# Kernel optimization log

Hardware: AMD Instinct MI355X
Metric: run time of the kernel (lower is better)

The kernel has to match this reference:

```python
import jax, jax.numpy as jnp
import numpy as np

B, T, D = 2, 2048, 2048
H, HD = 32, 64  # n_heads, head_dim; H*HD == attn_dim == D


def _rope(x, cos, sin):
    # x: (B,T,H,HD) with interleaved (real, imag) pairs on last dim
    b, t, h, hd = x.shape
    x2 = x.reshape(b, t, h, hd // 2, 2)
    xr, xi = x2[..., 0], x2[..., 1]
    c = cos[None, :, None, :]  # (1,T,1,HD/2)
    s = sin[None, :, None, :]
    out_r = xr * c - xi * s
    out_i = xr * s + xi * c
    return jnp.stack([out_r, out_i], axis=-1).reshape(b, t, h, hd)


def setup_inputs() -> dict:
    key = jax.random.key(0)
    ks = jax.random.split(key, 5)
    x = jax.random.normal(ks[0], (B, T, D), dtype=jnp.float32)
    scale = 0.02
    wq = jax.random.normal(ks[1], (D, D), dtype=jnp.float32) * scale
    wk = jax.random.normal(ks[2], (D, D), dtype=jnp.float32) * scale
    wv = jax.random.normal(ks[3], (D, D), dtype=jnp.float32) * scale
    wo = jax.random.normal(ks[4], (D, D), dtype=jnp.float32) * scale
    # standard RoPE frequencies, theta = 10000
    inv_freq = 1.0 / (10000.0 ** (jnp.arange(0, HD, 2, dtype=jnp.float32) / HD))  # (HD/2,)
    angles = jnp.arange(T, dtype=jnp.float32)[:, None] * inv_freq[None, :]  # (T, HD/2)
    return {
        "x": x,
        "freqs_cos": jnp.cos(angles),
        "freqs_sin": jnp.sin(angles),
        "wq": wq, "wk": wk, "wv": wv, "wo": wo,
    }


def reference(x, freqs_cos, freqs_sin, wq, wk, wv, wo):
    b, t, d = x.shape
    # fused-style QKV projections (nn.Linear: x @ W.T, no bias)
    q = (x @ wq.T).reshape(b, t, H, HD)
    k = (x @ wk.T).reshape(b, t, H, HD)
    v = (x @ wv.T).reshape(b, t, H, HD)
    q = _rope(q, freqs_cos, freqs_sin)
    k = _rope(k, freqs_cos, freqs_sin)
    # causal SDPA, scale = 1/sqrt(head_dim)
    scale = 1.0 / jnp.sqrt(jnp.float32(HD))
    scores = jnp.einsum("bqhd,bkhd->bhqk", q, k) * scale  # (B,H,T,T)
    causal = jnp.tril(jnp.ones((t, t), dtype=bool))
    scores = jnp.where(causal[None, None], scores, jnp.float32(-jnp.inf))
    attn = jax.nn.softmax(scores, axis=-1)
    y = jnp.einsum("bhqk,bkhd->bqhd", attn, v).reshape(b, t, H * HD)
    return y @ wo.T
```

## Files before the change

### kernel.cpp

```cpp
#include <hip/hip_runtime.h>
#include <hip/hip_bf16.h>
#include <stdint.h>


typedef __bf16 bf16_t;
typedef __bf16 bf16x4 __attribute__((ext_vector_type(4)));
typedef __bf16 bf16x8 __attribute__((ext_vector_type(8)));
typedef float  f32x4  __attribute__((ext_vector_type(4)));

constexpr int B_ = 2, T_ = 2048, D_ = 2048, H_ = 32, HD_ = 64;
constexpr int M_ = B_ * T_;

__device__ __forceinline__ void async_copy16(const bf16_t* g, bf16_t* l) {
  __builtin_amdgcn_global_load_lds(
      (const __attribute__((address_space(1))) void*)g,
      (__attribute__((address_space(3))) void*)l, 16, 0, 0);
}

__global__ __launch_bounds__(256) void cast_f32_bf16(
    const float* __restrict__ src, bf16_t* __restrict__ dst, int n4)
{
  const int i = blockIdx.x * 256 + threadIdx.x;
  if (i >= n4) return;
  const float4 v = ((const float4*)src)[i];
  bf16x4 o;
  o[0] = (bf16_t)v.x; o[1] = (bf16_t)v.y; o[2] = (bf16_t)v.z; o[3] = (bf16_t)v.w;
  ((bf16x4*)dst)[i] = o;
}

template <typename OutT>
__global__ __launch_bounds__(256, 2) void gemm_bt(
    const bf16_t* __restrict__ A, const bf16_t* __restrict__ B,
    OutT* __restrict__ C, int M, int N, int K)
{
  __shared__ __attribute__((aligned(16))) bf16_t As[128 * 32];
  __shared__ __attribute__((aligned(16))) bf16_t Bs[128 * 32];

  const int tid    = threadIdx.x;
  const int w      = tid >> 6;
  const int l      = tid & 63;
  const int quad   = l >> 4;
  const int lane16 = l & 15;
  const int bm0 = blockIdx.x * 128;
  const int bn0 = blockIdx.y * 128;
  const int wm  = (w >> 1) * 64;
  const int wn  = (w & 1) * 64;
  const int srow = l >> 2;
  const int scol = (l & 3) * 8;

  const bf16_t* Ag = A + (size_t)bm0 * K;
  const bf16_t* Bg = B + (size_t)bn0 * K;

  f32x4 acc[4][4] = {};

  for (int kk = 0; kk < K; kk += 32) {
    __syncthreads();
#pragma unroll
    for (int s0 = 0; s0 < 2; ++s0) {
      const int s = w + s0 * 4;
      async_copy16(Ag + (size_t)(s * 16 + srow) * K + kk + scol, &As[s * 512]);
      async_copy16(Bg + (size_t)(s * 16 + srow) * K + kk + scol, &Bs[s * 512]);
    }
    __syncthreads();

    bf16x8 af[4], bfr[4];
#pragma unroll
    for (int i = 0; i < 4; ++i)
      af[i] = *(const bf16x8*)&As[(wm + i * 16 + lane16) * 32 + quad * 8];
#pragma unroll
    for (int j = 0; j < 4; ++j)
      bfr[j] = *(const bf16x8*)&Bs[(wn + j * 16 + lane16) * 32 + quad * 8];
#pragma unroll
    for (int i = 0; i < 4; ++i)
#pragma unroll
      for (int j = 0; j < 4; ++j)
        acc[i][j] = __builtin_amdgcn_mfma_f32_16x16x32_bf16(af[i], bfr[j],
                                                            acc[i][j], 0, 0, 0);
  }

#pragma unroll
  for (int i = 0; i < 4; ++i) {
#pragma unroll
    for (int r = 0; r < 4; ++r) {
      const size_t row = (size_t)(bm0 + wm + i * 16 + quad * 4 + r);
#pragma unroll
      for (int j = 0; j < 4; ++j) {
        const int col = bn0 + wn + j * 16 + lane16;
        C[row * N + col] = (OutT)acc[i][j][r];
      }
    }
  }
}

__global__ __launch_bounds__(256, 2) void gemm_qkv(
    const bf16_t* __restrict__ A, const bf16_t* __restrict__ B,
    bf16_t* __restrict__ Cq, bf16_t* __restrict__ Ck, bf16_t* __restrict__ Cv,
    int M, int K)
{
  __shared__ __attribute__((aligned(16))) bf16_t As[128 * 32];
  __shared__ __attribute__((aligned(16))) bf16_t Bs[128 * 32];

  const int tid    = threadIdx.x;
  const int w      = tid >> 6;
  const int l      = tid & 63;
  const int quad   = l >> 4;
  const int lane16 = l & 15;
  const int bm0 = blockIdx.x * 128;
  const int bn0 = blockIdx.y * 128;
  const int wm  = (w >> 1) * 64;
  const int wn  = (w & 1) * 64;
  const int srow = l >> 2;
  const int scol = (l & 3) * 8;

  const bf16_t* Ag = A + (size_t)bm0 * K;
  const bf16_t* Bg = B + (size_t)bn0 * K;

  f32x4 acc[4][4] = {};

  for (int kk = 0; kk < K; kk += 32) {
    __syncthreads();
#pragma unroll
    for (int s0 = 0; s0 < 2; ++s0) {
      const int s = w + s0 * 4;
      async_copy16(Ag + (size_t)(s * 16 + srow) * K + kk + scol, &As[s * 512]);
      async_copy16(Bg + (size_t)(s * 16 + srow) * K + kk + scol, &Bs[s * 512]);
    }
    __syncthreads();

    bf16x8 af[4], bfr[4];
#pragma unroll
    for (int i = 0; i < 4; ++i)
      af[i] = *(const bf16x8*)&As[(wm + i * 16 + lane16) * 32 + quad * 8];
#pragma unroll
    for (int j = 0; j < 4; ++j)
      bfr[j] = *(const bf16x8*)&Bs[(wn + j * 16 + lane16) * 32 + quad * 8];
#pragma unroll
    for (int i = 0; i < 4; ++i)
#pragma unroll
      for (int j = 0; j < 4; ++j)
        acc[i][j] = __builtin_amdgcn_mfma_f32_16x16x32_bf16(af[i], bfr[j],
                                                            acc[i][j], 0, 0, 0);
  }

  bf16_t* Cb = (bn0 < 2048) ? Cq : (bn0 < 4096) ? Ck : Cv;
  const int cb0 = (bn0 & 2047) + wn;
#pragma unroll
  for (int i = 0; i < 4; ++i) {
#pragma unroll
    for (int r = 0; r < 4; ++r) {
      const size_t row = (size_t)(bm0 + wm + i * 16 + quad * 4 + r);
#pragma unroll
      for (int j = 0; j < 4; ++j)
        Cb[row * 2048 + cb0 + j * 16 + lane16] = (bf16_t)acc[i][j][r];
    }
  }
}

__global__ __launch_bounds__(256) void rope_kernel(
    bf16_t* __restrict__ q, bf16_t* __restrict__ k,
    const float* __restrict__ cosb, const float* __restrict__ sinb, int npair)
{
  const int idx = blockIdx.x * 256 + threadIdx.x;
  if (idx >= npair) return;
  const int p = idx & 31;
  const int t = (idx >> 10) & (T_ - 1);
  const float c = cosb[t * 32 + p];
  const float s = sinb[t * 32 + p];
  const size_t off = (size_t)idx * 2;

  const float qr = (float)q[off], qi = (float)q[off + 1];
  q[off]     = (bf16_t)((qr * c - qi * s) * 0.125f);
  q[off + 1] = (bf16_t)((qr * s + qi * c) * 0.125f);

  const float kr = (float)k[off], ki = (float)k[off + 1];
  k[off]     = (bf16_t)(kr * c - ki * s);
  k[off + 1] = (bf16_t)(kr * s + ki * c);
}

__global__ __launch_bounds__(256, 2) void flash_attn(
    const bf16_t* __restrict__ Q, const bf16_t* __restrict__ K,
    const bf16_t* __restrict__ V, bf16_t* __restrict__ Y)
{
  __shared__ __attribute__((aligned(16))) bf16_t Kf[4096];
  __shared__ __attribute__((aligned(16))) bf16_t Vf[4096];
  __shared__ __attribute__((aligned(16))) bf16_t Pt[4 * 2 * 16 * 68];

  const int tid    = threadIdx.x;
  const int w      = tid >> 6;
  const int l      = tid & 63;
  const int quad   = l >> 4;
  const int lane16 = l & 15;
  const int bh = blockIdx.y;
  const int b  = bh >> 5;
  const int h  = bh & 31;
  const int gx = blockIdx.x;
  int qa[2];
  qa[0] = gx * 128 + w * 32;
  qa[1] = (15 - gx) * 128 + w * 32;
  const size_t rs = (size_t)H_ * HD_;

  const bf16_t* Qb = Q + ((size_t)b * T_) * rs + h * HD_;
  const bf16_t* Kb = K + ((size_t)b * T_) * rs + h * HD_;
  const bf16_t* Vb = V + ((size_t)b * T_) * rs + h * HD_;

  bf16x8 qf[2][2][2];
#pragma unroll
  for (int g = 0; g < 2; ++g)
#pragma unroll
    for (int t = 0; t < 2; ++t)
#pragma unroll
      for (int c = 0; c < 2; ++c)
        qf[g][t][c] = *(const bf16x8*)(Qb + (size_t)(qa[g] + t * 16 + lane16) * rs +
                                       c * 32 + quad * 8);

  f32x4 o[2][2][4] = {};
  float lsum[2][2] = {};

  const int koff = tid >> 3;
  const int oct  = tid & 7;
  const int d0   = oct * 8;
  const int kc = oct >> 2, kq = oct & 3;
  const int nV = oct >> 1, base16 = (oct & 1) * 8;

  bf16_t* const PtW = Pt + w * (2 * 16 * 68);

  const int nsteps = (15 - gx) * 2 + 2;

  bf16x8 kr[2], vr[2];
#pragma unroll
  for (int hf = 0; hf < 2; ++hf) {
    const int key = hf * 32 + koff;
    kr[hf] = *(const bf16x8*)(Kb + (size_t)key * rs + d0);
    vr[hf] = *(const bf16x8*)(Vb + (size_t)key * rs + d0);
  }

  for (int it = 0; it < nsteps; ++it) {
    const int k0 = it * 64;
    __syncthreads();
#pragma unroll
    for (int hf = 0; hf < 2; ++hf) {
      const int key = hf * 32 + koff;
      const int gK = ((kc * 4 + (key >> 4)) * 16 + (key & 15)) * 4 + kq;
      *(bf16x8*)&Kf[gK * 8] = kr[hf];
      const int cV = key >> 5, qV = (key >> 3) & 3, jV = key & 7;
#pragma unroll
      for (int i = 0; i < 8; ++i) {
        const int gv = ((cV * 4 + nV) * 16 + base16 + i) * 4 + qV;
        Vf[(gv ^ oct) * 8 + jV] = vr[hf][i];
      }
    }
    __syncthreads();
    if (it + 1 < nsteps) {
      const int k0n = k0 + 64;
#pragma unroll
      for (int hf = 0; hf < 2; ++hf) {
        const int key = k0n + hf * 32 + koff;
        kr[hf] = *(const bf16x8*)(Kb + (size_t)key * rs + d0);
        vr[hf] = *(const bf16x8*)(Vb + (size_t)key * rs + d0);
      }
    }

#pragma unroll
    for (int g = 0; g < 2; ++g) {
      if (k0 > qa[g] + 31) continue;

      f32x4 stx[4][2] = {};
#pragma unroll
      for (int c = 0; c < 2; ++c) {
#pragma unroll
        for (int kt = 0; kt < 4; ++kt) {
          const bf16x8 kfr =
              *(const bf16x8*)&Kf[(((c * 4 + kt) * 16 + lane16) * 4 + quad) * 8];
          stx[kt][0] = __builtin_amdgcn_mfma_f32_16x16x32_bf16(kfr, qf[g][0][c],
                                                               stx[kt][0], 0, 0, 0);
          stx[kt][1] = __builtin_amdgcn_mfma_f32_16x16x32_bf16(kfr, qf[g][1][c],
                                                               stx[kt][1], 0, 0, 0);
        }
      }

#pragma unroll
      for (int t = 0; t < 2; ++t) {
        const int qbase = qa[g] + t * 16;
#pragma unroll
        for (int kt = 0; kt < 4; ++kt) {
          const int kbase = k0 + kt * 16 + quad * 4;
          const bool anymask = (k0 + kt * 16 + 15) > qbase;
          float p[4];
#pragma unroll
          for (int r = 0; r < 4; ++r) {
            float s = stx[kt][t][r];
            if (anymask) s = (kbase + r > qbase + lane16) ? -1e30f : s;
            p[r] = __expf(s);
          }
          lsum[g][t] += (p[0] + p[1]) + (p[2] + p[3]);
          bf16x4 pv;
          pv[0] = (bf16_t)p[0]; pv[1] = (bf16_t)p[1];
          pv[2] = (bf16_t)p[2]; pv[3] = (bf16_t)p[3];
          *(bf16x4*)&PtW[(t * 16 + lane16) * 68 + kt * 16 + quad * 4] = pv;
        }
      }

#pragma unroll
      for (int c = 0; c < 2; ++c) {
        const bf16x8 pf0 = *(const bf16x8*)&PtW[(0 * 16 + lane16) * 68 + c * 32 + quad * 8];
        const bf16x8 pf1 = *(const bf16x8*)&PtW[(1 * 16 + lane16) * 68 + c * 32 + quad * 8];
#pragma unroll
        for (int n = 0; n < 4; ++n) {
          const int gv = ((c * 4 + n) * 16 + lane16) * 4 + quad;
          const int swz = n * 2 + (lane16 >> 3);
          const bf16x8 vfr = *(const bf16x8*)&Vf[(gv ^ swz) * 8];
          o[g][0][n] = __builtin_amdgcn_mfma_f32_16x16x32_bf16(pf0, vfr, o[g][0][n], 0, 0, 0);
          o[g][1][n] = __builtin_amdgcn_mfma_f32_16x16x32_bf16(pf1, vfr, o[g][1][n], 0, 0, 0);
        }
      }
    }
  }

  bf16_t* Yb = Y + ((size_t)b * T_) * rs + h * HD_;
#pragma unroll
  for (int g = 0; g < 2; ++g) {
#pragma unroll
    for (int t = 0; t < 2; ++t) {
      float lt = lsum[g][t];
      lt += __shfl_xor(lt, 16);
      lt += __shfl_xor(lt, 32);
#pragma unroll
      for (int r = 0; r < 4; ++r) {
        const float linv = 1.0f / __shfl(lt, quad * 4 + r);
        const size_t row = (size_t)(qa[g] + t * 16 + quad * 4 + r);
#pragma unroll
        for (int n = 0; n < 4; ++n)
          Yb[row * rs + n * 16 + lane16] = (bf16_t)(o[g][t][n][r] * linv);
      }
    }
  }
}

extern "C" void kernel_launch(void* const* d_in, const int* in_sizes, int n_in,
                              void* d_out, int out_size, void* d_ws, size_t ws_size,
                              hipStream_t stream)
{
  (void)in_sizes; (void)n_in; (void)out_size;
  const float* x  = (const float*)d_in[0];
  const float* fc = (const float*)d_in[1];
  const float* fs = (const float*)d_in[2];
  const float* wq = (const float*)d_in[3];
  const float* wk = (const float*)d_in[4];
  const float* wv = (const float*)d_in[5];
  const float* wo = (const float*)d_in[6];
  float* out = (float*)d_out;

  const size_t nx = (size_t)M_ * D_;
  const size_t nw = (size_t)D_ * D_;
  const dim3 blk(256);
  const int nx4 = (int)(nx / 4), nw4 = (int)(nw / 4);
  const dim3 gg(M_ / 128, D_ / 128);

  if (ws_size >= (3 * nw + 4 * nx) * sizeof(bf16_t)) {
    bf16_t* ws  = (bf16_t*)d_ws;
    bf16_t* wb3 = ws;
    bf16_t* xb  = ws + 3 * nw;
    bf16_t* qb  = xb + nx;
    bf16_t* kb  = qb + nx;
    bf16_t* vb  = kb + nx;
    bf16_t* yb  = xb;

    cast_f32_bf16<<<dim3(nx4 / 256), blk, 0, stream>>>(x, xb, nx4);
    cast_f32_bf16<<<dim3(nw4 / 256), blk, 0, stream>>>(wq, wb3, nw4);
    cast_f32_bf16<<<dim3(nw4 / 256), blk, 0, stream>>>(wk, wb3 + nw, nw4);
    cast_f32_bf16<<<dim3(nw4 / 256), blk, 0, stream>>>(wv, wb3 + 2 * nw, nw4);

    gemm_qkv<<<dim3(M_ / 128, 48), blk, 0, stream>>>(xb, wb3, qb, kb, vb, M_, D_);

    rope_kernel<<<dim3((B_ * T_ * H_ * 32) / 256), blk, 0, stream>>>(
        qb, kb, fc, fs, B_ * T_ * H_ * 32);
    flash_attn<<<dim3(8, B_ * H_), blk, 0, stream>>>(qb, kb, vb, yb);

    cast_f32_bf16<<<dim3(nw4 / 256), blk, 0, stream>>>(wo, wb3, nw4);
    gemm_bt<float><<<gg, blk, 0, stream>>>(yb, wb3, out, M_, D_, D_);
  } else {
    bf16_t* ws = (bf16_t*)d_ws;
    bf16_t* wb = ws;
    bf16_t* xb = ws + nw;
    bf16_t* qb = xb + nx;
    bf16_t* kb = qb + nx;
    bf16_t* vb = kb + nx;
    bf16_t* yb = xb;

    cast_f32_bf16<<<dim3(nx4 / 256), blk, 0, stream>>>(x, xb, nx4);
    cast_f32_bf16<<<dim3(nw4 / 256), blk, 0, stream>>>(wq, wb, nw4);
    gemm_bt<bf16_t><<<gg, blk, 0, stream>>>(xb, wb, qb, M_, D_, D_);
    cast_f32_bf16<<<dim3(nw4 / 256), blk, 0, stream>>>(wk, wb, nw4);
    gemm_bt<bf16_t><<<gg, blk, 0, stream>>>(xb, wb, kb, M_, D_, D_);
    cast_f32_bf16<<<dim3(nw4 / 256), blk, 0, stream>>>(wv, wb, nw4);
    gemm_bt<bf16_t><<<gg, blk, 0, stream>>>(xb, wb, vb, M_, D_, D_);

    rope_kernel<<<dim3((B_ * T_ * H_ * 32) / 256), blk, 0, stream>>>(
        qb, kb, fc, fs, B_ * T_ * H_ * 32);
    flash_attn<<<dim3(8, B_ * H_), blk, 0, stream>>>(qb, kb, vb, yb);

    cast_f32_bf16<<<dim3(nw4 / 256), blk, 0, stream>>>(wo, wb, nw4);
    gemm_bt<float><<<gg, blk, 0, stream>>>(yb, wb, out, M_, D_, D_);
  }
}
```

Baseline: 413.5 us.

## Rewrite QKV GEMM as 256x256 pipelined tile kernel with fused RoPE epilogue

Replaces the 128x128 QKV projection GEMM with a 512-thread kernel that computes 256x256 tiles. It uses double-buffered async global-to-LDS loads over 64-wide K slices, a swizzled LDS layout, interleaved barrier-separated MFMA phases with raised wave priority, and a remapped block order for L2 locality. RoPE and the query scaling move into the GEMM epilogue through lane shuffles, which removes the separate rope kernel and its extra pass over Q and K. The cost is 128 KB of LDS per block and a fragile hand-written waitcnt and barrier schedule.

```diff
diff --git a/kernel.cpp b/kernel.cpp
--- a/kernel.cpp
+++ b/kernel.cpp
@@ -92,66 +92,199 @@
   }
 }
 
-__global__ __launch_bounds__(256, 2) void gemm_qkv(
-    const bf16_t* __restrict__ A, const bf16_t* __restrict__ B,
+template <int I0>
+__device__ __forceinline__ void rd4(const char* p, bf16x8 (&a)[4][2]) {
+#pragma unroll
+  for (int i = 0; i < 4; ++i)
+#pragma unroll
+    for (int ks = 0; ks < 2; ++ks)
+      a[i][ks] = *(const bf16x8*)(p + (((I0 + i) * 2 + ks) << 10));
+}
+
+template <int J0>
+__device__ __forceinline__ void rd2(const char* p, bf16x8 (&b)[2][2]) {
+#pragma unroll
+  for (int j = 0; j < 2; ++j)
+#pragma unroll
+    for (int ks = 0; ks < 2; ++ks)
+      b[j][ks] = *(const bf16x8*)(p + (((J0 + j) * 2 + ks) << 10));
+}
+
+template <int I0, int J0>
+__device__ __forceinline__ void mm16(f32x4 (&acc)[8][4],
+                                     const bf16x8 (&a)[4][2],
+                                     const bf16x8 (&b)[2][2]) {
+  __builtin_amdgcn_s_setprio(1);
+#pragma unroll
+  for (int i = 0; i < 4; ++i)
+#pragma unroll
+    for (int j = 0; j < 2; ++j)
+#pragma unroll
+      for (int ks = 0; ks < 2; ++ks)
+        acc[I0 + i][J0 + j] = __builtin_amdgcn_mfma_f32_16x16x32_bf16(
+            a[i][ks], b[j][ks], acc[I0 + i][J0 + j], 0, 0, 0);
+  __builtin_amdgcn_s_setprio(0);
+}
+
+#define GQ_BAR()   __builtin_amdgcn_s_barrier()
+#define GQ_LGKM0() asm volatile("s_waitcnt lgkmcnt(0)" ::: "memory")
+#define GQ_FENCE() asm volatile("" ::: "memory")
+
+__global__ __launch_bounds__(512, 2) void gemm_qkv8(
+    const bf16_t* __restrict__ A, const bf16_t* __restrict__ Bw,
     bf16_t* __restrict__ Cq, bf16_t* __restrict__ Ck, bf16_t* __restrict__ Cv,
-    int M, int K)
+    const float* __restrict__ fc, const float* __restrict__ fs)
 {
-  __shared__ __attribute__((aligned(16))) bf16_t As[128 * 32];
-  __shared__ __attribute__((aligned(16))) bf16_t Bs[128 * 32];
+  __shared__ __attribute__((aligned(16))) bf16_t lds[65536];
+  constexpr int K = 2048;
 
   const int tid    = threadIdx.x;
   const int w      = tid >> 6;
   const int l      = tid & 63;
   const int quad   = l >> 4;
   const int lane16 = l & 15;
-  const int bm0 = blockIdx.x * 128;
-  const int bn0 = blockIdx.y * 128;
-  const int wm  = (w >> 1) * 64;
-  const int wn  = (w & 1) * 64;
-  const int srow = l >> 2;
-  const int scol = (l & 3) * 8;
-
-  const bf16_t* Ag = A + (size_t)bm0 * K;
-  const bf16_t* Bg = B + (size_t)bn0 * K;
-
-  f32x4 acc[4][4] = {};
-
-  for (int kk = 0; kk < K; kk += 32) {
-    __syncthreads();
-#pragma unroll
-    for (int s0 = 0; s0 < 2; ++s0) {
-      const int s = w + s0 * 4;
-      async_copy16(Ag + (size_t)(s * 16 + srow) * K + kk + scol, &As[s * 512]);
-      async_copy16(Bg + (size_t)(s * 16 + srow) * K + kk + scol, &Bs[s * 512]);
-    }
-    __syncthreads();
-
-    bf16x8 af[4], bfr[4];
-#pragma unroll
-    for (int i = 0; i < 4; ++i)
-      af[i] = *(const bf16x8*)&As[(wm + i * 16 + lane16) * 32 + quad * 8];
-#pragma unroll
-    for (int j = 0; j < 4; ++j)
-      bfr[j] = *(const bf16x8*)&Bs[(wn + j * 16 + lane16) * 32 + quad * 8];
-#pragma unroll
-    for (int i = 0; i < 4; ++i)
-#pragma unroll
-      for (int j = 0; j < 4; ++j)
-        acc[i][j] = __builtin_amdgcn_mfma_f32_16x16x32_bf16(af[i], bfr[j],
-                                                            acc[i][j], 0, 0, 0);
-  }
-
-  bf16_t* Cb = (bn0 < 2048) ? Cq : (bn0 < 4096) ? Ck : Cv;
-  const int cb0 = (bn0 & 2047) + wn;
-#pragma unroll
-  for (int i = 0; i < 4; ++i) {
+  const int wr = w >> 2;
+  const int wc = w & 3;
+
+  const int lin = (blockIdx.x & 7) * 48 + (blockIdx.x >> 3);
+  const int bm0 = (lin & 15) << 8;
+  const int bn0 = (lin >> 4) << 8;
+
+  size_t so[2]; int lo[2];
+#pragma unroll
+  for (int c = 0; c < 2; ++c) {
+    const int g  = c * 512 + tid;
+    const int st = g >> 6, r4 = (g >> 2) & 15, cgs = g & 3;
+    const int cg = cgs ^ (((r4 >> 3) & 1) << 1);
+    so[c] = (size_t)(((st >> 1) << 4) + r4) * K + ((st & 1) << 5) + (cg << 3);
+    lo[c] = (c * 512 + (w << 6)) * 8;
+  }
+
+  const bf16_t* Ag = A  + (size_t)bm0 * K;
+  const bf16_t* Bg = Bw + (size_t)bn0 * K;
+
+  auto stA = [&](int half, int kt, int db) {
+    const bf16_t* gb = Ag + (size_t)(half << 7) * K + (kt << 6);
+    bf16_t* lb = &lds[((db << 1) + half) << 13];
+    async_copy16(gb + so[0], lb + lo[0]);
+    async_copy16(gb + so[1], lb + lo[1]);
+  };
+  auto stB = [&](int half, int kt, int db) {
+    const bf16_t* gb = Bg + (size_t)(half << 7) * K + (kt << 6);
+    bf16_t* lb = &lds[32768 + (((db << 1) + half) << 13)];
+    async_copy16(gb + so[0], lb + lo[0]);
+    async_copy16(gb + so[1], lb + lo[1]);
+  };
+
+  const int rbase = lane16 * 64 + ((quad ^ (((lane16 >> 3) & 1) << 1)) << 4);
+  const char* pAl = (const char*)lds + wr * 16384 + rbase;
+  const char* pBl = (const char*)lds + 65536 + ((wc >> 1) * 16384) +
+                    ((wc & 1) * 8192) + rbase;
+
+  f32x4 acc[8][4] = {};
+
+  stA(0, 0, 0); stA(1, 0, 0); stB(0, 0, 0); stB(1, 0, 0);
+  stA(0, 1, 1); stA(1, 1, 1);
+  asm volatile("s_waitcnt vmcnt(4)" ::: "memory");
+  GQ_BAR();
+  GQ_FENCE();
+
+#pragma unroll 1
+  for (int it = 0; it < 16; ++it) {
+    const int ktB = 2 * it + 1;
+    const int kt2 = (2 * it + 2 < 32) ? 2 * it + 2 : 31;
+    const int kt3 = (2 * it + 3 < 32) ? 2 * it + 3 : 31;
+    bf16x8 a0[4][2], a1[4][2], b0[2][2], b1[2][2];
+
+    rd4<0>(pAl, a0); rd2<0>(pBl, b0);
+    stB(0, ktB, 1);
+    asm volatile("s_waitcnt lgkmcnt(8)" ::: "memory");
+    GQ_BAR();
+    GQ_LGKM0();
+    mm16<0, 0>(acc, a0, b0);
+    GQ_BAR();
+
+    rd4<4>(pAl, a1);
+    stB(1, ktB, 1);
+    GQ_BAR();
+    GQ_LGKM0();
+    mm16<4, 0>(acc, a1, b0);
+    GQ_BAR();
+
+    rd2<2>(pBl, b1);
+    stA(0, kt2, 0);
+    GQ_BAR();
+    GQ_LGKM0();
+    mm16<0, 2>(acc, a0, b1);
+    GQ_BAR();
+
+    stA(1, kt2, 0);
+    GQ_BAR();
+    mm16<4, 2>(acc, a1, b1);
+    asm volatile("s_waitcnt vmcnt(4)" ::: "memory");
+    GQ_BAR();
+    GQ_FENCE();
+
+    const char* qAl = pAl + 32768;
+    const char* qBl = pBl + 32768;
+
+    rd4<0>(qAl, a0); rd2<0>(qBl, b0);
+    stB(0, kt2, 0);
+    asm volatile("s_waitcnt lgkmcnt(8)" ::: "memory");
+    GQ_BAR();
+    GQ_LGKM0();
+    mm16<0, 0>(acc, a0, b0);
+    GQ_BAR();
+
+    rd4<4>(qAl, a1);
+    stB(1, kt2, 0);
+    GQ_BAR();
+    GQ_LGKM0();
+    mm16<4, 0>(acc, a1, b0);
+    GQ_BAR();
+
+    rd2<2>(qBl, b1);
+    stA(0, kt3, 1);
+    GQ_BAR();
+    GQ_LGKM0();
+    mm16<0, 2>(acc, a0, b1);
+    GQ_BAR();
+
+    stA(1, kt3, 1);
+    GQ_BAR();
+    mm16<4, 2>(acc, a1, b1);
+    asm volatile("s_waitcnt vmcnt(4)" ::: "memory");
+    GQ_BAR();
+    GQ_FENCE();
+  }
+
+  asm volatile("s_waitcnt vmcnt(0)" ::: "memory");
+
+  bf16_t* Cb; float qs; int dorope;
+  if (bn0 < 2048)      { Cb = Cq; qs = 0.125f; dorope = 1; }
+  else if (bn0 < 4096) { Cb = Ck; qs = 1.0f;   dorope = 1; }
+  else                 { Cb = Cv; qs = 1.0f;   dorope = 0; }
+  const int cb0 = (bn0 & 2047) + (wc << 6);
+  const int rw0 = bm0 + wr * 128;
+
+#pragma unroll
+  for (int i = 0; i < 8; ++i) {
 #pragma unroll
     for (int r = 0; r < 4; ++r) {
-      const size_t row = (size_t)(bm0 + wm + i * 16 + quad * 4 + r);
-#pragma unroll
-      for (int j = 0; j < 4; ++j)
-        Cb[row * 2048 + cb0 + j * 16 + lane16] = (bf16_t)acc[i][j][r];
+      const int row = rw0 + i * 16 + quad * 4 + r;
+      const int t   = row & (T_ - 1);
+#pragma unroll
+      for (int j = 0; j < 4; ++j) {
+        float v = acc[i][j][r];
+        if (dorope) {
+          const int hd = j * 16 + lane16;
+          const float c  = fc[t * 32 + (hd >> 1)];
+          const float s  = fs[t * 32 + (hd >> 1)];
+          const float pr = __shfl_xor(v, 1);
+          v = ((hd & 1) ? (pr * s + v * c) : (v * c - pr * s)) * qs;
+        }
+        Cb[(size_t)row * 2048 + cb0 + j * 16 + lane16] = (bf16_t)v;
+      }
     }
   }
 }
@@ -370,10 +503,8 @@
     cast_f32_bf16<<<dim3(nw4 / 256), blk, 0, stream>>>(wk, wb3 + nw, nw4);
     cast_f32_bf16<<<dim3(nw4 / 256), blk, 0, stream>>>(wv, wb3 + 2 * nw, nw4);
 
-    gemm_qkv<<<dim3(M_ / 128, 48), blk, 0, stream>>>(xb, wb3, qb, kb, vb, M_, D_);
-
-    rope_kernel<<<dim3((B_ * T_ * H_ * 32) / 256), blk, 0, stream>>>(
-        qb, kb, fc, fs, B_ * T_ * H_ * 32);
+    gemm_qkv8<<<dim3(384), dim3(512), 0, stream>>>(xb, wb3, qb, kb, vb, fc, fs);
+
     flash_attn<<<dim3(8, B_ * H_), blk, 0, stream>>>(qb, kb, vb, yb);
 
     cast_f32_bf16<<<dim3(nw4 / 256), blk, 0, stream>>>(wo, wb3, nw4);
```

New measurement: 431.7 us. 4.4% more time.
